# Performance work log

Hardware: AMD Instinct MI355X
Metric: run time of the kernel (lower is better)

Reference implementation:

```python
import jax, jax.numpy as jnp
import numpy as np

B, M, RPI = 16, 80, 256            # images, objects/image, relations/image
N, R = B * M, B * RPI
DF, REP, EMB, HID, NH, L = 12544, 1024, 256, 512, 8, 4
OBJC, RELC = 151, 51
IMW, IMH = 800.0, 600.0


def _ln(x, g, b):
    m = x.mean(-1, keepdims=True)
    v = ((x - m) ** 2).mean(-1, keepdims=True)
    return (x - m) * jax.lax.rsqrt(v + 1e-5) * g + b


def _encoder(x, qkv_w, qkv_b, out_w, out_b, f1_w, f1_b, f2_w, f2_b, ln1_s, ln1_b, ln2_s, ln2_b):
    # post-LN transformer encoder, L layers, x: [B, M, HID]
    Bb, Mm, D = x.shape
    dk = D // NH
    scale = 1.0 / jnp.sqrt(jnp.float32(dk))
    for l in range(L):
        qkv = x @ qkv_w[l].T + qkv_b[l]
        q, k, v = jnp.split(qkv, 3, axis=-1)
        hs = lambda t: t.reshape(Bb, Mm, NH, dk).transpose(0, 2, 1, 3)
        q, k, v = hs(q), hs(k), hs(v)
        att = jax.nn.softmax(jnp.einsum('bhqd,bhkd->bhqk', q, k) * scale, axis=-1)
        o = jnp.einsum('bhqk,bhkd->bhqd', att, v).transpose(0, 2, 1, 3).reshape(Bb, Mm, D)
        x = _ln(x + o @ out_w[l].T + out_b[l], ln1_s[l], ln1_b[l])
        f = jax.nn.relu(x @ f1_w[l].T + f1_b[l]) @ f2_w[l].T + f2_b[l]
        x = _ln(x + f, ln2_s[l], ln2_b[l])
    return x


def _box_info(boxes):
    wh = boxes[:, 2:] - boxes[:, :2] + 1.0
    xy = boxes[:, :2] + 0.5 * wh
    w, h = wh[:, :1], wh[:, 1:]
    x, y = xy[:, :1], xy[:, 1:]
    x1, y1, x2, y2 = boxes[:, 0:1], boxes[:, 1:2], boxes[:, 2:3], boxes[:, 3:4]
    return jnp.concatenate([w / IMW, h / IMH, x / IMW, y / IMH, x1 / IMW, y1 / IMH,
                            x2 / IMW, y2 / IMH, w * h / (IMW * IMH)], axis=-1)  # [N, 9]


def setup_inputs() -> dict:
    key = jax.random.key(0)
    ks = iter(jax.random.split(key, 80))
    nrm = lambda shape, s=0.02: jax.random.normal(next(ks), shape, jnp.float32) * s
    d = {}
    d['features'] = jax.random.normal(next(ks), (N, DF), jnp.float32)
    d['union_features'] = jax.random.normal(next(ks), (R, REP), jnp.float32)
    x1 = jax.random.uniform(next(ks), (N, 1)) * (IMW - 120.0)
    y1 = jax.random.uniform(next(ks), (N, 1)) * (IMH - 120.0)
    w = jax.random.uniform(next(ks), (N, 1)) * 100.0 + 5.0
    h = jax.random.uniform(next(ks), (N, 1)) * 100.0 + 5.0
    d['boxes'] = jnp.concatenate([x1, y1, x1 + w, y1 + h], axis=-1)
    d['logits'] = jax.random.normal(next(ks), (N, OBJC), jnp.float32)
    d['labels'] = jax.random.randint(next(ks), (N,), 0, OBJC)
    d['rel_pair_idxs'] = jax.random.randint(next(ks), (B, RPI, 2), 0, M)
    # feature extractor
    d['fe1_w'] = nrm((REP, DF)); d['fe1_b'] = jnp.zeros((REP,))
    d['fe2_w'] = nrm((REP, REP)); d['fe2_b'] = jnp.zeros((REP,))
    # embeddings
    d['emb1'] = nrm((OBJC, EMB), 1.0)
    d['emb2'] = nrm((OBJC, EMB), 1.0)
    # bbox embed 9->32->128
    d['bb1_w'] = nrm((32, 9)); d['bb1_b'] = jnp.zeros((32,))
    d['bb2_w'] = nrm((128, 32)); d['bb2_b'] = jnp.zeros((128,))
    d['lobj_w'] = nrm((HID, REP + EMB + 128)); d['lobj_b'] = jnp.zeros((HID,))
    d['ledge_w'] = nrm((HID, EMB + HID)); d['ledge_b'] = jnp.zeros((HID,))
    for p in ('o', 'e'):
        d[p + 'qkv_w'] = nrm((L, 3 * HID, HID)); d[p + 'qkv_b'] = jnp.zeros((L, 3 * HID))
        d[p + 'out_w'] = nrm((L, HID, HID)); d[p + 'out_b'] = jnp.zeros((L, HID))
        d[p + 'f1_w'] = nrm((L, HID, HID)); d[p + 'f1_b'] = jnp.zeros((L, HID))
        d[p + 'f2_w'] = nrm((L, HID, HID)); d[p + 'f2_b'] = jnp.zeros((L, HID))
        d[p + 'ln1_s'] = jnp.ones((L, HID)); d[p + 'ln1_b'] = jnp.zeros((L, HID))
        d[p + 'ln2_s'] = jnp.ones((L, HID)); d[p + 'ln2_b'] = jnp.zeros((L, HID))
    d['pcat_w'] = nrm((REP, 2 * HID)); d['pcat_b'] = jnp.zeros((REP,))
    d['fuse_w'] = nrm((REP, REP + HID)); d['fuse_b'] = jnp.zeros((REP,))
    d['cpx_w'] = nrm((RELC, 2 * REP)); d['cpx_b'] = jnp.zeros((RELC,))
    d['dpath_w'] = nrm((RELC, REP)); d['dpath_b'] = jnp.zeros((RELC,))
    return d


def reference(features, union_features, boxes, logits,
              fe1_w, fe1_b, fe2_w, fe2_b, emb1, emb2,
              bb1_w, bb1_b, bb2_w, bb2_b, lobj_w, lobj_b, ledge_w, ledge_b,
              oqkv_w, oqkv_b, oout_w, oout_b, of1_w, of1_b, of2_w, of2_b,
              oln1_s, oln1_b, oln2_s, oln2_b,
              eqkv_w, eqkv_b, eout_w, eout_b, ef1_w, ef1_b, ef2_w, ef2_b,
              eln1_s, eln1_b, eln2_s, eln2_b,
              pcat_w, pcat_b, fuse_w, fuse_b, cpx_w, cpx_b, dpath_w, dpath_b,
              labels, rel_pair_idxs):
    # FeatureExtractor
    bf = jax.nn.relu(features @ fe1_w.T + fe1_b)
    bf = jax.nn.relu(bf @ fe2_w.T + fe2_b)                        # [N, REP]
    # bbox embedding (dropout = identity in eval)
    pos = jax.nn.relu(_box_info(boxes) @ bb1_w.T + bb1_b)
    pos = jax.nn.relu(pos @ bb2_w.T + bb2_b)                      # [N, 128]
    obj_rep = jnp.concatenate([bf, emb1[labels], pos], -1) @ lobj_w.T + lobj_b  # [N, HID]
    obj_emb = _encoder(obj_rep.reshape(B, M, HID), oqkv_w, oqkv_b, oout_w, oout_b,
                       of1_w, of1_b, of2_w, of2_b, oln1_s, oln1_b, oln2_s, oln2_b)  # [B, M, HID]
    edge_in = jnp.concatenate([obj_emb.reshape(N, HID), emb2[labels]], -1) @ ledge_w.T + ledge_b
    gctx = _encoder(edge_in.reshape(B, M, HID), eqkv_w, eqkv_b, eout_w, eout_b,
                    ef1_w, ef1_b, ef2_w, ef2_b, eln1_s, eln1_b, eln2_s, eln2_b).mean(axis=1)  # [B, HID]
    # pair gather per image
    head = jax.vmap(lambda e, i: e[i])(obj_emb, rel_pair_idxs[:, :, 0])  # [B, RPI, HID]
    tail = jax.vmap(lambda e, i: e[i])(obj_emb, rel_pair_idxs[:, :, 1])
    pair = jnp.concatenate([head, tail], -1).reshape(R, 2 * HID)
    local = pair @ pcat_w.T + pcat_b                               # [R, REP]
    gexp = jnp.repeat(gctx, RPI, axis=0)                           # [R, HID]
    sem = jax.nn.relu(jnp.concatenate([local, gexp], -1) @ fuse_w.T + fuse_b)
    final = jnp.concatenate([sem, union_features], -1)             # [R, 2*REP]
    rel_logits = final @ cpx_w.T + cpx_b + local @ dpath_w.T + dpath_b  # [R, RELC]
    return rel_logits
```

## Files before the change

### kernel.cpp

```cpp
#include <hip/hip_runtime.h>
#include <hip/hip_bf16.h>
#include <cstdint>

#define DEV_INLINE __device__ __forceinline__

using u16 = unsigned short;
typedef __attribute__((ext_vector_type(8))) short bf8_t;
typedef __attribute__((ext_vector_type(4))) float f32x4;

constexpr int cB = 16, cM = 80, cRPI = 256;
constexpr int cN = cB * cM;
constexpr int cR = cB * cRPI;
constexpr int cDF = 12544, cREP = 1024, cEMB = 256, cHID = 512, cNH = 8, cL = 4;
constexpr int cRELC = 51;

DEV_INLINE u16 f2bf(float x) { return __builtin_bit_cast(u16, __float2bfloat16(x)); }
DEV_INLINE float bf2f(u16 u) { return __bfloat162float(__builtin_bit_cast(__hip_bfloat16, u)); }

DEV_INLINE float wave_max(float v) {
#pragma unroll
  for (int o = 32; o; o >>= 1) v = fmaxf(v, __shfl_xor(v, o));
  return v;
}
DEV_INLINE float wave_sum(float v) {
#pragma unroll
  for (int o = 32; o; o >>= 1) v += __shfl_xor(v, o);
  return v;
}

DEV_INLINE void xcd_remap(int& bx, int& by) {
  const int gx = gridDim.x;
  const int nwg = gx * gridDim.y;
  const int id = blockIdx.x + gx * blockIdx.y;
  const int q = nwg >> 3, r = nwg & 7;
  const int x = id & 7, k = id >> 3;
  const int idp = (x < r) ? x * (q + 1) + k : r * (q + 1) + (x - r) * q + k;
  bx = idp % gx;
  by = idp / gx;
}

template <int KK>
__global__ __launch_bounds__(256) void gemm_k1(
    const u16* __restrict__ A, int lda,
    const u16* __restrict__ Bw, int ldb,
    float* __restrict__ outF, int ldc,
    u16* __restrict__ outH, int ldh,
    const float* __restrict__ bias,
    const float* __restrict__ res, int resld, int resmode,
    int relu)
{
  constexpr int GR = KK / 8;
  constexpr int CH = 32 * GR;
  __shared__ u16 As[32 * KK];
  __shared__ u16 Bs[32 * KK];
  const int tid = threadIdx.x;
  const int wid = tid >> 6, lane = tid & 63;
  const int l15 = lane & 15, l4 = lane >> 4;
  int bx, by;
  xcd_remap(bx, by);
  const int bm = by * 32, bn = bx * 32;
  const int wr = wid >> 1, wc = wid & 1;

#pragma unroll
  for (int i = 0; i < CH / 256; ++i) {
    const int c = i * 256 + tid;
    const int row = c / GR, gran = c % GR;
    const int sg = gran ^ (row & 7);
    const u16* gp = A + (size_t)(bm + row) * lda + sg * 8;
    __builtin_amdgcn_global_load_lds(
        (const __attribute__((address_space(1))) void*)gp,
        (__attribute__((address_space(3))) void*)((char*)As + (size_t)(i * 256 + wid * 64) * 16),
        16, 0, 0);
  }
#pragma unroll
  for (int i = 0; i < CH / 256; ++i) {
    const int c = i * 256 + tid;
    const int row = c / GR, gran = c % GR;
    const int sg = gran ^ (row & 7);
    const u16* gp = Bw + (size_t)(bn + row) * ldb + sg * 8;
    __builtin_amdgcn_global_load_lds(
        (const __attribute__((address_space(1))) void*)gp,
        (__attribute__((address_space(3))) void*)((char*)Bs + (size_t)(i * 256 + wid * 64) * 16),
        16, 0, 0);
  }
  __syncthreads();

  const int ra = wr * 16 + l15;
  const int rb = wc * 16 + l15;
  f32x4 acc = {};
#pragma unroll
  for (int ks = 0; ks < KK / 32; ++ks) {
    const int ga = ((ks << 2) | l4) ^ (ra & 7);
    const int gb = ((ks << 2) | l4) ^ (rb & 7);
    const bf8_t af = *(const bf8_t*)&As[ra * KK + ga * 8];
    const bf8_t bv = *(const bf8_t*)&Bs[rb * KK + gb * 8];
    acc = __builtin_amdgcn_mfma_f32_16x16x32_bf16(af, bv, acc, 0, 0, 0);
  }

  const int ccol = bn + wc * 16 + l15;
  const float bv = bias ? bias[ccol] : 0.f;
#pragma unroll
  for (int g = 0; g < 4; ++g) {
    const int r = bm + wr * 16 + l4 * 4 + g;
    float v = acc[g] + bv;
    if (resmode == 1) v += res[(size_t)r * resld + ccol];
    else if (resmode == 2) v += res[(size_t)(r >> 8) * resld + ccol];
    if (relu) v = fmaxf(v, 0.f);
    if (outF) outF[(size_t)r * ldc + ccol] = v;
    if (outH) outH[(size_t)r * ldh + ccol] = f2bf(v);
  }
}

static void g512(hipStream_t s, const u16* A, int lda, const u16* W, int ldb,
                 int M, int N, float* outF, int ldc, u16* outH, int ldh,
                 const float* bias, const float* res, int resld, int resmode, int relu) {
  dim3 g(N / 32, M / 32);
  gemm_k1<512><<<g, 256, 0, s>>>(A, lda, W, ldb, outF, ldc, outH, ldh,
                                 bias, res, resld, resmode, relu);
}

template <int BM, int BN, bool SPLIT>
__global__ __launch_bounds__(256) void gemm_h(
    const u16* __restrict__ A, int lda,
    const u16* __restrict__ Bw, int ldb,
    int Mr, int Nr, int Klen,
    float* __restrict__ outF, int ldc,
    u16* __restrict__ outH, int ldh,
    const float* __restrict__ bias,
    const float* __restrict__ res, int resld, int resmode,
    int relu)
{
  constexpr int MF = BM > 32 ? BM / 32 : 1, NF = BN > 32 ? BN / 32 : 1;
  constexpr int ACH = BM * 4, BCH = BN * 4;
  __shared__ u16 As[2][BM * 32];
  __shared__ u16 Bs[2][BN * 32];
  const int tid = threadIdx.x;
  const int wid = tid >> 6, lane = tid & 63;
  const int l15 = lane & 15, l4 = lane >> 4;
  int bx, by;
  xcd_remap(bx, by);
  const int bm = by * BM, bn = bx * BN;
  const int wr = wid >> 1, wc = wid & 1;
  const int kbase = SPLIT ? blockIdx.z * Klen : 0;

  f32x4 acc[MF][NF] = {};

  auto stage = [&](int buf, int ks) {
    const int k0 = kbase + (ks << 5);
#pragma unroll
    for (int i = 0; i < (ACH + 255) / 256; ++i) {
      const int cA = i * 256 + tid;
      if (ACH % 256 == 0 || cA < ACH) {
        const int row = cA >> 2, seg = cA & 3;
        const int sseg = seg ^ (row & 3);
        const u16* gp = A + (size_t)(bm + row) * lda + k0 + sseg * 8;
        __builtin_amdgcn_global_load_lds(
            (const __attribute__((address_space(1))) void*)gp,
            (__attribute__((address_space(3))) void*)((char*)As[buf] + (size_t)(cA - lane) * 16),
            16, 0, 0);
      }
    }
#pragma unroll
    for (int i = 0; i < (BCH + 255) / 256; ++i) {
      const int cBp = i * 256 + ((tid + 128) & 255);
      if (BCH % 256 == 0 || cBp < BCH) {
        const int row = cBp >> 2, seg = cBp & 3;
        const int sseg = seg ^ (row & 3);
        int brow = bn + row; if (brow > Nr - 1) brow = Nr - 1;
        const u16* gp = Bw + (size_t)brow * ldb + k0 + sseg * 8;
        __builtin_amdgcn_global_load_lds(
            (const __attribute__((address_space(1))) void*)gp,
            (__attribute__((address_space(3))) void*)((char*)Bs[buf] + (size_t)(cBp - lane) * 16),
            16, 0, 0);
      }
    }
  };

  const int nk = Klen >> 5;
  stage(0, 0);
  __syncthreads();

  for (int ks = 0; ks < nk; ++ks) {
    const int cur = ks & 1;
    if (ks + 1 < nk) stage(cur ^ 1, ks + 1);

    bf8_t af[MF], bfr[NF];
#pragma unroll
    for (int m = 0; m < MF; ++m) {
      const int r = wr * (BM / 2) + m * 16 + l15;
      const int g = l4 ^ (r & 3);
      af[m] = *(const bf8_t*)&As[cur][r * 32 + g * 8];
    }
#pragma unroll
    for (int n = 0; n < NF; ++n) {
      const int r = wc * (BN / 2) + n * 16 + l15;
      const int g = l4 ^ (r & 3);
      bfr[n] = *(const bf8_t*)&Bs[cur][r * 32 + g * 8];
    }
#pragma unroll
    for (int m = 0; m < MF; ++m)
#pragma unroll
      for (int n = 0; n < NF; ++n)
        acc[m][n] = __builtin_amdgcn_mfma_f32_16x16x32_bf16(af[m], bfr[n], acc[m][n], 0, 0, 0);
    __syncthreads();
  }

  if (SPLIT) {
    float* po = outF + (size_t)blockIdx.z * Mr * ldc;
#pragma unroll
    for (int m = 0; m < MF; ++m)
#pragma unroll
      for (int n = 0; n < NF; ++n) {
        const int ccol = bn + wc * (BN / 2) + n * 16 + l15;
        if (ccol >= Nr) continue;
#pragma unroll
        for (int g = 0; g < 4; ++g) {
          const int r = bm + wr * (BM / 2) + m * 16 + l4 * 4 + g;
          po[(size_t)r * ldc + ccol] = acc[m][n][g];
        }
      }
  } else {
#pragma unroll
    for (int m = 0; m < MF; ++m)
#pragma unroll
      for (int n = 0; n < NF; ++n) {
        const int ccol = bn + wc * (BN / 2) + n * 16 + l15;
        if (ccol >= Nr) continue;
        const float bv = bias ? bias[ccol] : 0.f;
#pragma unroll
        for (int g = 0; g < 4; ++g) {
          const int r = bm + wr * (BM / 2) + m * 16 + l4 * 4 + g;
          float v = acc[m][n][g] + bv;
          if (resmode == 1) v += res[(size_t)r * resld + ccol];
          else if (resmode == 2) v += res[(size_t)(r >> 8) * resld + ccol];
          if (relu) v = fmaxf(v, 0.f);
          if (outF) outF[(size_t)r * ldc + ccol] = v;
          if (outH) outH[(size_t)r * ldh + ccol] = f2bf(v);
        }
      }
  }
}

template <int BM, int BN>
static void g16(hipStream_t s, const u16* A, int lda, const u16* W, int ldb,
                int M, int N, int K, float* outF, int ldc, u16* outH, int ldh,
                const float* bias, const float* res, int resld, int resmode, int relu) {
  dim3 g((N + BN - 1) / BN, M / BM);
  gemm_h<BM, BN, false><<<g, 256, 0, s>>>(A, lda, W, ldb, M, N, K, outF, ldc, outH, ldh,
                                          bias, res, resld, resmode, relu);
}

__global__ void conv_big2(const float* __restrict__ f, const float* __restrict__ w,
                          u16* __restrict__ fh, u16* __restrict__ wh) {
  constexpr int N1 = cN * cDF / 4;
  constexpr int N2 = cREP * cDF / 4;
  for (int i = blockIdx.x * 256 + threadIdx.x; i < N1 + N2; i += gridDim.x * 256) {
    const float4 v = (i < N1) ? ((const float4*)f)[i] : ((const float4*)w)[i - N1];
    ushort4 o = {f2bf(v.x), f2bf(v.y), f2bf(v.z), f2bf(v.w)};
    if (i < N1) ((ushort4*)fh)[i] = o; else ((ushort4*)wh)[i - N1] = o;
  }
}

constexpr size_t W_FE2 = 0, W_LOBJ = W_FE2 + 1048576, W_LEDGE = W_LOBJ + 720896,
  W_OQKV = W_LEDGE + 393216, W_OOUT = W_OQKV + 3145728, W_OF1 = W_OOUT + 1048576,
  W_OF2 = W_OF1 + 1048576, W_EQKV = W_OF2 + 1048576, W_EOUT = W_EQKV + 3145728,
  W_EF1 = W_EOUT + 1048576, W_EF2 = W_EF1 + 1048576, W_PCAT = W_EF2 + 1048576,
  W_FUSE = W_PCAT + 1048576, W_WEND = W_FUSE + 1572864;

struct EncSrcs {
  const float *fe2, *lobj, *ledge, *oqkv, *oout, *of1, *of2,
              *eqkv, *eout, *ef1, *ef2, *pcat, *fuse;
};

__global__ void conv_enc(EncSrcs S, u16* __restrict__ wb) {
#define SEG(nm, OFF, PRE, LEN) \
  if (i < (PRE) + (LEN)) { \
    const float4 v = ((const float4*)S.nm)[i - (PRE)]; \
    ushort4 o = {f2bf(v.x), f2bf(v.y), f2bf(v.z), f2bf(v.w)}; \
    ((ushort4*)(wb + (OFF)))[i - (PRE)] = o; \
  } else
  for (int i = blockIdx.x * 256 + threadIdx.x; i < (int)(W_WEND / 4); i += gridDim.x * 256) {
    SEG(fe2,  W_FE2,   0,       262144)
    SEG(lobj, W_LOBJ,  262144,  180224)
    SEG(ledge,W_LEDGE, 442368,  98304)
    SEG(oqkv, W_OQKV,  540672,  786432)
    SEG(oout, W_OOUT,  1327104, 262144)
    SEG(of1,  W_OF1,   1589248, 262144)
    SEG(of2,  W_OF2,   1851392, 262144)
    SEG(eqkv, W_EQKV,  2113536, 786432)
    SEG(eout, W_EOUT,  2899968, 262144)
    SEG(ef1,  W_EF1,   3162112, 262144)
    SEG(ef2,  W_EF2,   3424256, 262144)
    SEG(pcat, W_PCAT,  3686400, 262144)
    SEG(fuse, W_FUSE,  3948544, 393216)
    { }
  }
#undef SEG
}

__global__ void conv_cat(const float* __restrict__ cpx, const float* __restrict__ dpath,
                         const float* __restrict__ cb, const float* __restrict__ db,
                         u16* __restrict__ catw, float* __restrict__ biasc) {
  constexpr int N1 = cRELC * 512;
  constexpr int N2 = cRELC * 256;
  const int i0 = blockIdx.x * 256 + threadIdx.x;
  if (blockIdx.x == 0 && threadIdx.x < cRELC) biasc[threadIdx.x] = cb[threadIdx.x] + db[threadIdx.x];
  for (int i = i0; i < N1 + N2; i += gridDim.x * 256) {
    if (i < N1) {
      const int r = i >> 9, c = i & 511;
      const float4 v = ((const float4*)cpx)[i];
      ushort4 o = {f2bf(v.x), f2bf(v.y), f2bf(v.z), f2bf(v.w)};
      ((ushort4*)catw)[r * 768 + c] = o;
    } else {
      const int j = i - N1, r = j >> 8, c = j & 255;
      const float4 v = ((const float4*)dpath)[j];
      ushort4 o = {f2bf(v.x), f2bf(v.y), f2bf(v.z), f2bf(v.w)};
      ((ushort4*)catw)[r * 768 + 512 + c] = o;
    }
  }
}

__global__ void conv2d_kernel(const float* __restrict__ src, int slda,
                              u16* __restrict__ dst, int dld, int cols) {
  const int r = blockIdx.x;
  for (int c = threadIdx.x; c < cols; c += blockDim.x)
    dst[(size_t)r * dld + c] = f2bf(src[(size_t)r * slda + c]);
}

__global__ __launch_bounds__(256) void prep_obj(
    const float* __restrict__ boxes,
    const float* __restrict__ bb1w, const float* __restrict__ bb1b,
    const float* __restrict__ bb2w, const float* __restrict__ bb2b,
    const float* __restrict__ emb1, const int* __restrict__ labels,
    u16* __restrict__ obj_in) {
  __shared__ float W1[288];
  __shared__ float W2[4096];
  __shared__ float P1[8][33];
  const int tid = threadIdx.x;
  for (int i = tid; i < 288; i += 256) W1[i] = bb1w[i];
  for (int i = tid; i < 4096; i += 256) W2[i] = bb2w[i];
  __syncthreads();
  const int r8 = tid >> 5, sub = tid & 31;
  const int row = blockIdx.x * 8 + r8;
  const float x1 = boxes[row * 4], y1 = boxes[row * 4 + 1];
  const float x2 = boxes[row * 4 + 2], y2 = boxes[row * 4 + 3];
  const float w = x2 - x1 + 1.f, h = y2 - y1 + 1.f;
  const float bi[9] = {w / 800.f, h / 600.f, (x1 + 0.5f * w) / 800.f, (y1 + 0.5f * h) / 600.f,
                       x1 / 800.f, y1 / 600.f, x2 / 800.f, y2 / 600.f, w * h / 480000.f};
  float p = bb1b[sub];
#pragma unroll
  for (int j = 0; j < 9; ++j) p += bi[j] * W1[sub * 9 + j];
  P1[r8][sub] = fmaxf(p, 0.f);
  __syncthreads();
#pragma unroll
  for (int jo = 0; jo < 4; ++jo) {
    const int o = sub + jo * 32;
    float a = bb2b[o];
#pragma unroll
    for (int j2 = 0; j2 < 32; ++j2) a += P1[r8][j2] * W2[o * 32 + j2];
    obj_in[(size_t)row * 1408 + 1280 + o] = f2bf(fmaxf(a, 0.f));
  }
  const int l = labels[row];
#pragma unroll
  for (int k = 0; k < 8; ++k)
    obj_in[(size_t)row * 1408 + 1024 + sub + k * 32] = f2bf(emb1[(size_t)l * 256 + sub + k * 32]);
}

__global__ void gather_emb_h(const float* __restrict__ emb, const int* __restrict__ labels,
                             u16* __restrict__ dst, int dld) {
  const int i = blockIdx.x;
  const int l = labels[i];
  const float* s = emb + (size_t)l * cEMB;
  for (int c = threadIdx.x; c < cEMB; c += blockDim.x)
    dst[(size_t)i * dld + c] = f2bf(s[c]);
}

__global__ __launch_bounds__(256) void attn_kernel(const u16* __restrict__ qkv,
                                                   u16* __restrict__ o) {
  __shared__ float Ks[80][65];
  __shared__ float Vs[80][65];
  const int bh = blockIdx.x;
  const int b = bh >> 3, h = bh & 7;
  const int tid = threadIdx.x;
  const u16* base = qkv + (size_t)(b * cM) * 1536 + h * 64;

  for (int e = tid; e < 640; e += 256) {
    const int r = e >> 3, d0 = (e & 7) * 8;
    const bf8_t kv = *(const bf8_t*)&base[(size_t)r * 1536 + 512 + d0];
    const bf8_t vv = *(const bf8_t*)&base[(size_t)r * 1536 + 1024 + d0];
#pragma unroll
    for (int j = 0; j < 8; ++j) {
      Ks[r][d0 + j] = bf2f((u16)kv[j]);
      Vs[r][d0 + j] = bf2f((u16)vv[j]);
    }
  }
  __syncthreads();

  const int wave = tid >> 6, lane = tid & 63;
  const int r0 = blockIdx.y * 16;
  for (int r = r0 + wave; r < r0 + 16; r += 4) {
    const float qd = bf2f(base[(size_t)r * 1536 + lane]);
    const int c2 = 64 + lane;
    const int c2c = (c2 < 80) ? c2 : 0;
    float s0 = 0.f, s1 = 0.f;
#pragma unroll 8
    for (int d = 0; d < 64; ++d) {
      const float qv = __shfl(qd, d);
      s0 += qv * Ks[lane][d];
      s1 += qv * Ks[c2c][d];
    }
    s0 *= 0.125f;
    s1 = (c2 < 80) ? s1 * 0.125f : -1e30f;
    const float mx = wave_max(fmaxf(s0, s1));
    const float p0 = __expf(s0 - mx);
    const float p1 = (c2 < 80) ? __expf(s1 - mx) : 0.f;
    const float ssum = wave_sum(p0 + p1);

    float od = 0.f;
#pragma unroll 8
    for (int c = 0; c < 64; ++c) od += __shfl(p0, c) * Vs[c][lane];
#pragma unroll
    for (int c = 0; c < 16; ++c) od += __shfl(p1, c) * Vs[64 + c][lane];
    od /= ssum;
    o[(size_t)(b * cM + r) * cHID + h * 64 + lane] = f2bf(od);
  }
}

__global__ __launch_bounds__(256) void ln_kernel(
    const float* __restrict__ in, float* __restrict__ outF,
    u16* __restrict__ outH, int ldh,
    const float* __restrict__ g, const float* __restrict__ bta) {
  const int row = blockIdx.x * 4 + (threadIdx.x >> 6);
  const int lane = threadIdx.x & 63;
  const float* x = in + (size_t)row * cHID;
  float v[8];
  float s = 0.f;
#pragma unroll
  for (int i = 0; i < 8; ++i) { v[i] = x[lane + i * 64]; s += v[i]; }
  s = wave_sum(s);
  const float mean = s * (1.f / 512.f);
  float vs = 0.f;
#pragma unroll
  for (int i = 0; i < 8; ++i) { const float d = v[i] - mean; vs += d * d; }
  vs = wave_sum(vs);
  const float inv = rsqrtf(vs * (1.f / 512.f) + 1e-5f);
#pragma unroll
  for (int i = 0; i < 8; ++i) {
    const int c = lane + i * 64;
    const float y = (v[i] - mean) * inv * g[c] + bta[c];
    outF[(size_t)row * cHID + c] = y;
    outH[(size_t)row * ldh + c] = f2bf(y);
  }
}

__global__ void mean_kernel(const float* __restrict__ x, u16* __restrict__ gctx_h) {
  const int b = blockIdx.x;
  const int c = threadIdx.x;
  float s = 0.f;
  for (int m = 0; m < cM; ++m) s += x[(size_t)(b * cM + m) * cHID + c];
  gctx_h[(size_t)b * cHID + c] = f2bf(s * (1.f / 80.f));
}

__global__ void pair_gather_h(const u16* __restrict__ obj, int old, const int* __restrict__ idx,
                              u16* __restrict__ pair) {
  const int r = blockIdx.x;
  const int b = r >> 8, rr = r & 255;
  const int i0 = idx[(size_t)(b * cRPI + rr) * 2 + 0];
  const int i1 = idx[(size_t)(b * cRPI + rr) * 2 + 1];
  const u16* hsrc = obj + (size_t)(b * cM + i0) * old;
  const u16* tsrc = obj + (size_t)(b * cM + i1) * old;
  u16* p = pair + (size_t)r * 1024;
  for (int c = threadIdx.x; c < cHID; c += blockDim.x) {
    p[c] = hsrc[c];
    p[cHID + c] = tsrc[c];
  }
}

__global__ void reduce8_kernel(const float* __restrict__ p, const float* __restrict__ bias,
                               u16* __restrict__ outH) {
  const int idx = blockIdx.x * 256 + threadIdx.x;
  constexpr int total = cN * cREP;
  if (idx >= total) return;
  float v = bias[idx & 1023];
#pragma unroll
  for (int z = 0; z < 8; ++z) v += p[(size_t)z * total + idx];
  outH[idx] = f2bf(fmaxf(v, 0.f));
}

__global__ void freduce_kernel(const float* __restrict__ p, const float* __restrict__ biasc,
                               float* __restrict__ out) {
  const int idx = blockIdx.x * 256 + threadIdx.x;
  if (idx >= cR * cRELC) return;
  const int r = idx / cRELC, c = idx - r * cRELC;
  float v = biasc[c];
#pragma unroll
  for (int z = 0; z < 4; ++z) v += p[(size_t)z * cR * 64 + (size_t)r * 64 + c];
  out[idx] = v;
}

static void run_encoder(hipStream_t s, float* x, u16* xh, u16* qkvh, u16* attn_h,
                        float* res1, u16* f_h,
                        const u16* qkvw, const float* qkvb,
                        const u16* outw, const float* outb,
                        const u16* f1w, const float* f1b,
                        const u16* f2w, const float* f2b,
                        const float* ln1s, const float* ln1b,
                        const float* ln2s, const float* ln2b,
                        u16* last_bf, int last_ld) {
  for (int l = 0; l < cL; ++l) {
    g512(s, xh, 512, qkvw + (size_t)l * 1536 * 512, 512, cN, 1536,
         nullptr, 0, qkvh, 1536, qkvb + l * 1536, nullptr, 0, 0, 0);
    attn_kernel<<<dim3(cB * cNH, 5), 256, 0, s>>>(qkvh, attn_h);
    g512(s, attn_h, 512, outw + (size_t)l * 512 * 512, 512, cN, 512,
         res1, 512, nullptr, 0, outb + l * 512, x, 512, 1, 0);
    ln_kernel<<<cN / 4, 256, 0, s>>>(res1, x, xh, 512, ln1s + l * 512, ln1b + l * 512);
    g512(s, xh, 512, f1w + (size_t)l * 512 * 512, 512, cN, 512,
         nullptr, 0, f_h, 512, f1b + l * 512, nullptr, 0, 0, 1);
    g512(s, f_h, 512, f2w + (size_t)l * 512 * 512, 512, cN, 512,
         res1, 512, nullptr, 0, f2b + l * 512, x, 512, 1, 0);
    const bool last = (l == cL - 1);
    ln_kernel<<<cN / 4, 256, 0, s>>>(res1, x, last ? last_bf : xh, last ? last_ld : 512,
                                     ln2s + l * 512, ln2b + l * 512);
  }
}

constexpr size_t OFF_FEAT  = 0;
constexpr size_t OFF_FE1W  = 32112640;
constexpr size_t OFF_PART  = 57802752;
constexpr size_t P_END     = 99745792;
constexpr size_t OFF_PAIR  = 0;
constexpr size_t OFF_FINAL = 8388608;
constexpr size_t OFF_OBJIN = 33554432;
constexpr size_t OFF_QKVH  = 37158912;
constexpr size_t OFF_X     = 41091072;
constexpr size_t OFF_XH    = 43712512;
constexpr size_t OFF_ATTN  = 45023232;
constexpr size_t OFF_RES   = 46333952;
constexpr size_t OFF_FH    = 48955392;
constexpr size_t OFF_EDGE  = 50266112;

extern "C" void kernel_launch(void* const* d_in, const int* in_sizes, int n_in,
                              void* d_out, int out_size, void* d_ws, size_t ws_size,
                              hipStream_t stream) {
  (void)in_sizes; (void)n_in; (void)out_size; (void)ws_size;

  const float* features = (const float*)d_in[0];
  const float* unionf   = (const float*)d_in[1];
  const float* boxes    = (const float*)d_in[2];
  const int*   labels   = (const int*)d_in[4];
  const int*   relidx   = (const int*)d_in[5];
  const float* fe1_w = (const float*)d_in[6];
  const float* fe1_b = (const float*)d_in[7];
  const float* fe2_w = (const float*)d_in[8];
  const float* fe2_b = (const float*)d_in[9];
  const float* emb1  = (const float*)d_in[10];
  const float* emb2  = (const float*)d_in[11];
  const float* bb1_w = (const float*)d_in[12];
  const float* bb1_b = (const float*)d_in[13];
  const float* bb2_w = (const float*)d_in[14];
  const float* bb2_b = (const float*)d_in[15];
  const float* lobj_w = (const float*)d_in[16];
  const float* lobj_b = (const float*)d_in[17];
  const float* ledge_w = (const float*)d_in[18];
  const float* ledge_b = (const float*)d_in[19];
  const float* oqkv_w = (const float*)d_in[20];
  const float* oqkv_b = (const float*)d_in[21];
  const float* oout_w = (const float*)d_in[22];
  const float* oout_b = (const float*)d_in[23];
  const float* of1_w = (const float*)d_in[24];
  const float* of1_b = (const float*)d_in[25];
  const float* of2_w = (const float*)d_in[26];
  const float* of2_b = (const float*)d_in[27];
  const float* oln1_s = (const float*)d_in[28];
  const float* oln1_b = (const float*)d_in[29];
  const float* oln2_s = (const float*)d_in[30];
  const float* oln2_b = (const float*)d_in[31];
  const float* eqkv_w = (const float*)d_in[32];
  const float* eqkv_b = (const float*)d_in[33];
  const float* eout_w = (const float*)d_in[34];
  const float* eout_b = (const float*)d_in[35];
  const float* ef1_w = (const float*)d_in[36];
  const float* ef1_b = (const float*)d_in[37];
  const float* ef2_w = (const float*)d_in[38];
  const float* ef2_b = (const float*)d_in[39];
  const float* eln1_s = (const float*)d_in[40];
  const float* eln1_b = (const float*)d_in[41];
  const float* eln2_s = (const float*)d_in[42];
  const float* eln2_b = (const float*)d_in[43];
  const float* pcat_w = (const float*)d_in[44];
  const float* pcat_b = (const float*)d_in[45];
  const float* fuse_w = (const float*)d_in[46];
  const float* fuse_b = (const float*)d_in[47];
  const float* cpx_w  = (const float*)d_in[48];
  const float* cpx_b  = (const float*)d_in[49];
  const float* dpath_w = (const float*)d_in[50];
  const float* dpath_b = (const float*)d_in[51];

  char* wsb = (char*)d_ws;
  u16* feat_h  = (u16*)(wsb + OFF_FEAT);
  u16* fe1w_h  = (u16*)(wsb + OFF_FE1W);
  float* part  = (float*)(wsb + OFF_PART);
  u16* pair    = (u16*)(wsb + OFF_PAIR);
  u16* finalb  = (u16*)(wsb + OFF_FINAL);
  u16* obj_in  = (u16*)(wsb + OFF_OBJIN);
  u16* qkvh    = (u16*)(wsb + OFF_QKVH);
  float* x     = (float*)(wsb + OFF_X);
  u16* xh      = (u16*)(wsb + OFF_XH);
  u16* attn_h  = (u16*)(wsb + OFF_ATTN);
  float* res1  = (float*)(wsb + OFF_RES);
  u16* f_h     = (u16*)(wsb + OFF_FH);
  u16* edge_in = (u16*)(wsb + OFF_EDGE);

  size_t off = P_END;
  auto alloc = [&](size_t bytes) { char* p = wsb + off; off = (off + bytes + 255) & ~(size_t)255; return p; };
  u16* wblock   = (u16*)alloc(W_WEND * 2);
  u16* catw     = (u16*)alloc(313344);
  float* biasc  = (float*)alloc(256);
  u16* bf0h     = (u16*)alloc(2621440);
  u16* gctx_h   = (u16*)alloc(65536);
  float* gcproj = (float*)alloc(262144);
  float* fpart  = (float*)alloc(4194304);

  const u16* fe2w_h   = wblock + W_FE2;
  const u16* lobjw_h  = wblock + W_LOBJ;
  const u16* ledgew_h = wblock + W_LEDGE;
  const u16* oqkvw_h  = wblock + W_OQKV;
  const u16* ooutw_h  = wblock + W_OOUT;
  const u16* of1w_h   = wblock + W_OF1;
  const u16* of2w_h   = wblock + W_OF2;
  const u16* eqkvw_h  = wblock + W_EQKV;
  const u16* eoutw_h  = wblock + W_EOUT;
  const u16* ef1w_h   = wblock + W_EF1;
  const u16* ef2w_h   = wblock + W_EF2;
  const u16* pcatw_h  = wblock + W_PCAT;
  const u16* fusew_h  = wblock + W_FUSE;

  conv_big2<<<2048, 256, 0, stream>>>(features, fe1_w, feat_h, fe1w_h);
  EncSrcs es = {fe2_w, lobj_w, ledge_w, oqkv_w, oout_w, of1_w, of2_w,
                eqkv_w, eout_w, ef1_w, ef2_w, pcat_w, fuse_w};
  conv_enc<<<2048, 256, 0, stream>>>(es, wblock);
  conv_cat<<<160, 256, 0, stream>>>(cpx_w, dpath_w, cpx_b, dpath_b, catw, biasc);

  gemm_h<128, 128, true><<<dim3(8, 10, 8), 256, 0, stream>>>(
      feat_h, cDF, fe1w_h, cDF, cN, cREP, cDF / 8, part, cREP,
      nullptr, 0, nullptr, nullptr, 0, 0, 0);
  reduce8_kernel<<<(cN * cREP + 255) / 256, 256, 0, stream>>>(part, fe1_b, bf0h);

  prep_obj<<<cN / 8, 256, 0, stream>>>(boxes, bb1_w, bb1_b, bb2_w, bb2_b, emb1, labels, obj_in);

  g16<32, 32>(stream, bf0h, 1024, fe2w_h, 1024, cN, cREP, cREP,
              nullptr, 0, obj_in, 1408, fe2_b, nullptr, 0, 0, 1);

  g16<32, 32>(stream, obj_in, 1408, lobjw_h, 1408, cN, cHID, 1408,
              x, 512, xh, 512, lobj_b, nullptr, 0, 0, 0);

  run_encoder(stream, x, xh, qkvh, attn_h, res1, f_h,
              oqkvw_h, oqkv_b, ooutw_h, oout_b, of1w_h, of1_b, of2w_h, of2_b,
              oln1_s, oln1_b, oln2_s, oln2_b, edge_in, 768);

  gather_emb_h<<<cN, 256, 0, stream>>>(emb2, labels, edge_in + 512, 768);
  pair_gather_h<<<cR, 256, 0, stream>>>(edge_in, 768, relidx, pair);

  g16<32, 32>(stream, edge_in, 768, ledgew_h, 768, cN, cHID, 768,
              x, 512, xh, 512, ledge_b, nullptr, 0, 0, 0);
  run_encoder(stream, x, xh, qkvh, attn_h, res1, f_h,
              eqkvw_h, eqkv_b, eoutw_h, eout_b, ef1w_h, ef1_b, ef2w_h, ef2_b,
              eln1_s, eln1_b, eln2_s, eln2_b, xh, 512);
  mean_kernel<<<cB, cHID, 0, stream>>>(x, gctx_h);

  g512(stream, gctx_h, 512, fusew_h + 1024, 1536, 64, cREP,
       gcproj, 1024, nullptr, 0, fuse_b, nullptr, 0, 0, 0);

  conv2d_kernel<<<cR, 256, 0, stream>>>(unionf, 1024, finalb + 1024, 3072, 1024);
  g16<128, 64>(stream, pair, 1024, pcatw_h, 1024, cR, cREP, 1024,
               nullptr, 0, finalb + 2048, 3072, pcat_b, nullptr, 0, 0, 0);
  g16<128, 64>(stream, finalb + 2048, 3072, fusew_h, 1536, cR, cREP, 1024,
               nullptr, 0, finalb, 3072, nullptr, gcproj, 1024, 2, 1);

  gemm_h<64, 64, true><<<dim3(1, 64, 4), 256, 0, stream>>>(
      finalb, 3072, catw, 3072, cR, cRELC, 3072 / 4, fpart, 64,
      nullptr, 0, nullptr, nullptr, 0, 0, 0);
  freduce_kernel<<<(cR * cRELC + 255) / 256, 256, 0, stream>>>(fpart, biasc, (float*)d_out);
}
```

Measured before the change: 879.7 us.

## Fuse LayerNorm into encoder GEMMs and merge conversion and gather kernels

Adds a gemm_ln kernel that applies LayerNorm on the fly, either normalizing the A operand (with per-row stats computed in-kernel) or normalizing the residual in the epilogue. The encoder no longer launches separate ln_kernel passes except at the last layer, and it shifts the next layer's QKV projection to consume the LN2 output directly. It also merges the three weight/feature conversion kernels into one launch, and the embedding gather with the pair gather. This is meant to cut launch count and the round trips of normalized activations through memory. The cost is that LN statistics are recomputed per column-tile block, using a one-pass variance formula.

```diff
diff --git a/kernel.cpp b/kernel.cpp
--- a/kernel.cpp
+++ b/kernel.cpp
@@ -26,6 +26,12 @@
 #pragma unroll
   for (int o = 32; o; o >>= 1) v += __shfl_xor(v, o);
   return v;
+}
+
+DEV_INLINE void gl_lds16(const u16* gp, char* lp) {
+  __builtin_amdgcn_global_load_lds(
+      (const __attribute__((address_space(1))) void*)gp,
+      (__attribute__((address_space(3))) void*)lp, 16, 0, 0);
 }
 
 DEV_INLINE void xcd_remap(int& bx, int& by) {
@@ -37,6 +43,129 @@
   const int idp = (x < r) ? x * (q + 1) + k : r * (q + 1) + (x - r) * q + k;
   bx = idp % gx;
   by = idp / gx;
+}
+
+template <int LNA, int LNRES>
+__global__ __launch_bounds__(256) void gemm_ln(
+    const u16* __restrict__ Ah,
+    const float* __restrict__ Sres,
+    const float* __restrict__ lnS, const float* __restrict__ lnB,
+    const u16* __restrict__ W,
+    float* __restrict__ outF,
+    u16* __restrict__ outH, int ldh,
+    const float* __restrict__ bias, int relu)
+{
+  __shared__ u16 As[32 * 512];
+  __shared__ u16 Bs[32 * 512];
+  __shared__ float stat[32][2];
+  const int tid = threadIdx.x;
+  const int wid = tid >> 6, lane = tid & 63;
+  const int l15 = lane & 15, l4 = lane >> 4;
+  int bx, by;
+  xcd_remap(bx, by);
+  const int bm = by * 32, bn = bx * 32;
+  const int wr = wid >> 1, wc = wid & 1;
+
+#pragma unroll
+  for (int i = 0; i < 8; ++i) {
+    const int c = i * 256 + tid;
+    const int row = c >> 6, gran = c & 63;
+    const int sg = gran ^ (row & 7);
+    gl_lds16(W + (size_t)(bn + row) * 512 + sg * 8,
+             (char*)Bs + (size_t)(i * 256 + wid * 64) * 16);
+  }
+
+  if (LNA) {
+    const int r8 = tid >> 3, sub = tid & 7;
+    const float4* rp4 = (const float4*)(Sres + (size_t)(bm + r8) * 512 + sub * 64);
+    float4 v[16];
+    float s = 0.f, q = 0.f;
+#pragma unroll
+    for (int k = 0; k < 16; ++k) {
+      v[k] = rp4[k];
+      s += v[k].x + v[k].y + v[k].z + v[k].w;
+      q += v[k].x * v[k].x + v[k].y * v[k].y + v[k].z * v[k].z + v[k].w * v[k].w;
+    }
+#pragma unroll
+    for (int o = 1; o < 8; o <<= 1) { s += __shfl_xor(s, o); q += __shfl_xor(q, o); }
+    const float mean = s * (1.f / 512.f);
+    const float inv = rsqrtf(q * (1.f / 512.f) - mean * mean + 1e-5f);
+    if (sub == 0) { stat[r8][0] = mean; stat[r8][1] = inv; }
+    const float4* ls4 = (const float4*)(lnS + sub * 64);
+    const float4* lb4 = (const float4*)(lnB + sub * 64);
+#pragma unroll
+    for (int k2 = 0; k2 < 8; ++k2) {
+      const float4 a = v[k2 * 2], b = v[k2 * 2 + 1];
+      const float4 sa = ls4[k2 * 2], sb = ls4[k2 * 2 + 1];
+      const float4 ba = lb4[k2 * 2], bb = lb4[k2 * 2 + 1];
+      bf8_t wv;
+      wv[0] = (short)f2bf((a.x - mean) * inv * sa.x + ba.x);
+      wv[1] = (short)f2bf((a.y - mean) * inv * sa.y + ba.y);
+      wv[2] = (short)f2bf((a.z - mean) * inv * sa.z + ba.z);
+      wv[3] = (short)f2bf((a.w - mean) * inv * sa.w + ba.w);
+      wv[4] = (short)f2bf((b.x - mean) * inv * sb.x + bb.x);
+      wv[5] = (short)f2bf((b.y - mean) * inv * sb.y + bb.y);
+      wv[6] = (short)f2bf((b.z - mean) * inv * sb.z + bb.z);
+      wv[7] = (short)f2bf((b.w - mean) * inv * sb.w + bb.w);
+      const int g = sub * 8 + k2;
+      const int sg = g ^ (r8 & 7);
+      *(bf8_t*)&As[r8 * 512 + sg * 8] = wv;
+    }
+  } else {
+#pragma unroll
+    for (int i = 0; i < 8; ++i) {
+      const int c = i * 256 + tid;
+      const int row = c >> 6, gran = c & 63;
+      const int sg = gran ^ (row & 7);
+      gl_lds16(Ah + (size_t)(bm + row) * 512 + sg * 8,
+               (char*)As + (size_t)(i * 256 + wid * 64) * 16);
+    }
+    if (LNRES) {
+      const int r8 = tid >> 3, sub = tid & 7;
+      const float4* rp4 = (const float4*)(Sres + (size_t)(bm + r8) * 512 + sub * 64);
+      float s = 0.f, q = 0.f;
+#pragma unroll
+      for (int k = 0; k < 16; ++k) {
+        const float4 t = rp4[k];
+        s += t.x + t.y + t.z + t.w;
+        q += t.x * t.x + t.y * t.y + t.z * t.z + t.w * t.w;
+      }
+#pragma unroll
+      for (int o = 1; o < 8; o <<= 1) { s += __shfl_xor(s, o); q += __shfl_xor(q, o); }
+      const float mean = s * (1.f / 512.f);
+      const float inv = rsqrtf(q * (1.f / 512.f) - mean * mean + 1e-5f);
+      if (sub == 0) { stat[r8][0] = mean; stat[r8][1] = inv; }
+    }
+  }
+  __syncthreads();
+
+  const int ra = wr * 16 + l15;
+  const int rbr = wc * 16 + l15;
+  f32x4 acc = {};
+#pragma unroll
+  for (int ks = 0; ks < 16; ++ks) {
+    const int ga = ((ks << 2) | l4) ^ (ra & 7);
+    const int gb = ((ks << 2) | l4) ^ (rbr & 7);
+    const bf8_t af = *(const bf8_t*)&As[ra * 512 + ga * 8];
+    const bf8_t bv = *(const bf8_t*)&Bs[rbr * 512 + gb * 8];
+    acc = __builtin_amdgcn_mfma_f32_16x16x32_bf16(af, bv, acc, 0, 0, 0);
+  }
+
+  const int ccol = bn + wc * 16 + l15;
+  const float bv = bias[ccol];
+  float rs = 0.f, rbb = 0.f;
+  if (LNRES) { rs = lnS[ccol]; rbb = lnB[ccol]; }
+#pragma unroll
+  for (int g = 0; g < 4; ++g) {
+    const int rl = wr * 16 + l4 * 4 + g;
+    const int r = bm + rl;
+    float vv = acc[g] + bv;
+    if (LNRES)
+      vv += (Sres[(size_t)r * 512 + ccol] - stat[rl][0]) * stat[rl][1] * rs + rbb;
+    if (relu) vv = fmaxf(vv, 0.f);
+    if (outF) outF[(size_t)r * 512 + ccol] = vv;
+    if (outH) outH[(size_t)r * ldh + ccol] = f2bf(vv);
+  }
 }
 
 template <int KK>
@@ -66,22 +195,16 @@
     const int c = i * 256 + tid;
     const int row = c / GR, gran = c % GR;
     const int sg = gran ^ (row & 7);
-    const u16* gp = A + (size_t)(bm + row) * lda + sg * 8;
-    __builtin_amdgcn_global_load_lds(
-        (const __attribute__((address_space(1))) void*)gp,
-        (__attribute__((address_space(3))) void*)((char*)As + (size_t)(i * 256 + wid * 64) * 16),
-        16, 0, 0);
+    gl_lds16(A + (size_t)(bm + row) * lda + sg * 8,
+             (char*)As + (size_t)(i * 256 + wid * 64) * 16);
   }
 #pragma unroll
   for (int i = 0; i < CH / 256; ++i) {
     const int c = i * 256 + tid;
     const int row = c / GR, gran = c % GR;
     const int sg = gran ^ (row & 7);
-    const u16* gp = Bw + (size_t)(bn + row) * ldb + sg * 8;
-    __builtin_amdgcn_global_load_lds(
-        (const __attribute__((address_space(1))) void*)gp,
-        (__attribute__((address_space(3))) void*)((char*)Bs + (size_t)(i * 256 + wid * 64) * 16),
-        16, 0, 0);
+    gl_lds16(Bw + (size_t)(bn + row) * ldb + sg * 8,
+             (char*)Bs + (size_t)(i * 256 + wid * 64) * 16);
   }
   __syncthreads();
 
@@ -153,11 +276,8 @@
       if (ACH % 256 == 0 || cA < ACH) {
         const int row = cA >> 2, seg = cA & 3;
         const int sseg = seg ^ (row & 3);
-        const u16* gp = A + (size_t)(bm + row) * lda + k0 + sseg * 8;
-        __builtin_amdgcn_global_load_lds(
-            (const __attribute__((address_space(1))) void*)gp,
-            (__attribute__((address_space(3))) void*)((char*)As[buf] + (size_t)(cA - lane) * 16),
-            16, 0, 0);
+        gl_lds16(A + (size_t)(bm + row) * lda + k0 + sseg * 8,
+                 (char*)As[buf] + (size_t)(cA - lane) * 16);
       }
     }
 #pragma unroll
@@ -167,11 +287,8 @@
         const int row = cBp >> 2, seg = cBp & 3;
         const int sseg = seg ^ (row & 3);
         int brow = bn + row; if (brow > Nr - 1) brow = Nr - 1;
-        const u16* gp = Bw + (size_t)brow * ldb + k0 + sseg * 8;
-        __builtin_amdgcn_global_load_lds(
-            (const __attribute__((address_space(1))) void*)gp,
-            (__attribute__((address_space(3))) void*)((char*)Bs[buf] + (size_t)(cBp - lane) * 16),
-            16, 0, 0);
+        gl_lds16(Bw + (size_t)brow * ldb + k0 + sseg * 8,
+                 (char*)Bs[buf] + (size_t)(cBp - lane) * 16);
       }
     }
   };
@@ -250,74 +367,61 @@
                                           bias, res, resld, resmode, relu);
 }
 
-__global__ void conv_big2(const float* __restrict__ f, const float* __restrict__ w,
-                          u16* __restrict__ fh, u16* __restrict__ wh) {
-  constexpr int N1 = cN * cDF / 4;
-  constexpr int N2 = cREP * cDF / 4;
-  for (int i = blockIdx.x * 256 + threadIdx.x; i < N1 + N2; i += gridDim.x * 256) {
-    const float4 v = (i < N1) ? ((const float4*)f)[i] : ((const float4*)w)[i - N1];
-    ushort4 o = {f2bf(v.x), f2bf(v.y), f2bf(v.z), f2bf(v.w)};
-    if (i < N1) ((ushort4*)fh)[i] = o; else ((ushort4*)wh)[i - N1] = o;
-  }
-}
-
 constexpr size_t W_FE2 = 0, W_LOBJ = W_FE2 + 1048576, W_LEDGE = W_LOBJ + 720896,
   W_OQKV = W_LEDGE + 393216, W_OOUT = W_OQKV + 3145728, W_OF1 = W_OOUT + 1048576,
   W_OF2 = W_OF1 + 1048576, W_EQKV = W_OF2 + 1048576, W_EOUT = W_EQKV + 3145728,
   W_EF1 = W_EOUT + 1048576, W_EF2 = W_EF1 + 1048576, W_PCAT = W_EF2 + 1048576,
   W_FUSE = W_PCAT + 1048576, W_WEND = W_FUSE + 1572864;
 
-struct EncSrcs {
+struct ConvAll {
+  const float *features, *fe1w;
   const float *fe2, *lobj, *ledge, *oqkv, *oout, *of1, *of2,
               *eqkv, *eout, *ef1, *ef2, *pcat, *fuse;
+  const float *cpx, *dpath, *cb, *db;
+  u16 *feat_h, *fe1w_h, *wb, *catw;
+  float *biasc;
 };
 
-__global__ void conv_enc(EncSrcs S, u16* __restrict__ wb) {
-#define SEG(nm, OFF, PRE, LEN) \
+__global__ void conv_all(ConvAll C) {
+  if (blockIdx.x == 0 && threadIdx.x < cRELC)
+    C.biasc[threadIdx.x] = C.cb[threadIdx.x] + C.db[threadIdx.x];
+#define CSEG(src, dst, PRE, LEN) \
   if (i < (PRE) + (LEN)) { \
-    const float4 v = ((const float4*)S.nm)[i - (PRE)]; \
+    const float4 v = ((const float4*)(src))[i - (PRE)]; \
     ushort4 o = {f2bf(v.x), f2bf(v.y), f2bf(v.z), f2bf(v.w)}; \
-    ((ushort4*)(wb + (OFF)))[i - (PRE)] = o; \
+    ((ushort4*)(dst))[i - (PRE)] = o; \
   } else
-  for (int i = blockIdx.x * 256 + threadIdx.x; i < (int)(W_WEND / 4); i += gridDim.x * 256) {
-    SEG(fe2,  W_FE2,   0,       262144)
-    SEG(lobj, W_LOBJ,  262144,  180224)
-    SEG(ledge,W_LEDGE, 442368,  98304)
-    SEG(oqkv, W_OQKV,  540672,  786432)
-    SEG(oout, W_OOUT,  1327104, 262144)
-    SEG(of1,  W_OF1,   1589248, 262144)
-    SEG(of2,  W_OF2,   1851392, 262144)
-    SEG(eqkv, W_EQKV,  2113536, 786432)
-    SEG(eout, W_EOUT,  2899968, 262144)
-    SEG(ef1,  W_EF1,   3162112, 262144)
-    SEG(ef2,  W_EF2,   3424256, 262144)
-    SEG(pcat, W_PCAT,  3686400, 262144)
-    SEG(fuse, W_FUSE,  3948544, 393216)
-    { }
-  }
-#undef SEG
-}
-
-__global__ void conv_cat(const float* __restrict__ cpx, const float* __restrict__ dpath,
-                         const float* __restrict__ cb, const float* __restrict__ db,
-                         u16* __restrict__ catw, float* __restrict__ biasc) {
-  constexpr int N1 = cRELC * 512;
-  constexpr int N2 = cRELC * 256;
-  const int i0 = blockIdx.x * 256 + threadIdx.x;
-  if (blockIdx.x == 0 && threadIdx.x < cRELC) biasc[threadIdx.x] = cb[threadIdx.x] + db[threadIdx.x];
-  for (int i = i0; i < N1 + N2; i += gridDim.x * 256) {
-    if (i < N1) {
-      const int r = i >> 9, c = i & 511;
-      const float4 v = ((const float4*)cpx)[i];
+  for (int i = blockIdx.x * 256 + threadIdx.x; i < 11606272; i += gridDim.x * 256) {
+    CSEG(C.features, C.feat_h,      0,        4014080)
+    CSEG(C.fe1w,     C.fe1w_h,      4014080,  3211264)
+    CSEG(C.fe2,      C.wb + W_FE2,  7225344,  262144)
+    CSEG(C.lobj,     C.wb + W_LOBJ, 7487488,  180224)
+    CSEG(C.ledge,    C.wb + W_LEDGE,7667712,  98304)
+    CSEG(C.oqkv,     C.wb + W_OQKV, 7766016,  786432)
+    CSEG(C.oout,     C.wb + W_OOUT, 8552448,  262144)
+    CSEG(C.of1,      C.wb + W_OF1,  8814592,  262144)
+    CSEG(C.of2,      C.wb + W_OF2,  9076736,  262144)
+    CSEG(C.eqkv,     C.wb + W_EQKV, 9338880,  786432)
+    CSEG(C.eout,     C.wb + W_EOUT, 10125312, 262144)
+    CSEG(C.ef1,      C.wb + W_EF1,  10387456, 262144)
+    CSEG(C.ef2,      C.wb + W_EF2,  10649600, 262144)
+    CSEG(C.pcat,     C.wb + W_PCAT, 10911744, 262144)
+    CSEG(C.fuse,     C.wb + W_FUSE, 11173888, 393216)
+    if (i < 11593216) {
+      const int j = i - 11567104;
+      const int r = j >> 9, c = j & 511;
+      const float4 v = ((const float4*)C.cpx)[j];
       ushort4 o = {f2bf(v.x), f2bf(v.y), f2bf(v.z), f2bf(v.w)};
-      ((ushort4*)catw)[r * 768 + c] = o;
+      ((ushort4*)C.catw)[r * 768 + c] = o;
     } else {
-      const int j = i - N1, r = j >> 8, c = j & 255;
-      const float4 v = ((const float4*)dpath)[j];
+      const int j = i - 11593216;
+      const int r = j >> 8, c = j & 255;
+      const float4 v = ((const float4*)C.dpath)[j];
       ushort4 o = {f2bf(v.x), f2bf(v.y), f2bf(v.z), f2bf(v.w)};
-      ((ushort4*)catw)[r * 768 + 512 + c] = o;
-    }
-  }
+      ((ushort4*)C.catw)[r * 768 + 512 + c] = o;
+    }
+  }
+#undef CSEG
 }
 
 __global__ void conv2d_kernel(const float* __restrict__ src, int slda,
@@ -366,13 +470,25 @@
     obj_in[(size_t)row * 1408 + 1024 + sub + k * 32] = f2bf(emb1[(size_t)l * 256 + sub + k * 32]);
 }
 
-__global__ void gather_emb_h(const float* __restrict__ emb, const int* __restrict__ labels,
-                             u16* __restrict__ dst, int dld) {
-  const int i = blockIdx.x;
-  const int l = labels[i];
-  const float* s = emb + (size_t)l * cEMB;
-  for (int c = threadIdx.x; c < cEMB; c += blockDim.x)
-    dst[(size_t)i * dld + c] = f2bf(s[c]);
+__global__ void gather_pair(const float* __restrict__ emb2, const int* __restrict__ labels,
+                            u16* __restrict__ edge_in,
+                            const int* __restrict__ idx, u16* __restrict__ pair) {
+  const int r = blockIdx.x;
+  const int tid = threadIdx.x;
+  if (r < cN && tid < cEMB) {
+    const int l = labels[r];
+    edge_in[(size_t)r * 768 + 512 + tid] = f2bf(emb2[(size_t)l * cEMB + tid]);
+  }
+  const int b = r >> 8, rr = r & 255;
+  const int i0 = idx[(size_t)(b * cRPI + rr) * 2 + 0];
+  const int i1 = idx[(size_t)(b * cRPI + rr) * 2 + 1];
+  const u16* hsrc = edge_in + (size_t)(b * cM + i0) * 768;
+  const u16* tsrc = edge_in + (size_t)(b * cM + i1) * 768;
+  u16* p = pair + (size_t)r * 1024;
+  for (int c = tid; c < cHID; c += blockDim.x) {
+    p[c] = hsrc[c];
+    p[cHID + c] = tsrc[c];
+  }
 }
 
 __global__ __launch_bounds__(256) void attn_kernel(const u16* __restrict__ qkv,
@@ -461,21 +577,6 @@
   gctx_h[(size_t)b * cHID + c] = f2bf(s * (1.f / 80.f));
 }
 
-__global__ void pair_gather_h(const u16* __restrict__ obj, int old, const int* __restrict__ idx,
-                              u16* __restrict__ pair) {
-  const int r = blockIdx.x;
-  const int b = r >> 8, rr = r & 255;
-  const int i0 = idx[(size_t)(b * cRPI + rr) * 2 + 0];
-  const int i1 = idx[(size_t)(b * cRPI + rr) * 2 + 1];
-  const u16* hsrc = obj + (size_t)(b * cM + i0) * old;
-  const u16* tsrc = obj + (size_t)(b * cM + i1) * old;
-  u16* p = pair + (size_t)r * 1024;
-  for (int c = threadIdx.x; c < cHID; c += blockDim.x) {
-    p[c] = hsrc[c];
-    p[cHID + c] = tsrc[c];
-  }
-}
-
 __global__ void reduce8_kernel(const float* __restrict__ p, const float* __restrict__ bias,
                                u16* __restrict__ outH) {
   const int idx = blockIdx.x * 256 + threadIdx.x;
@@ -499,7 +600,7 @@
 }
 
 static void run_encoder(hipStream_t s, float* x, u16* xh, u16* qkvh, u16* attn_h,
-                        float* res1, u16* f_h,
+                        float* res1, float* res2, u16* f_h,
                         const u16* qkvw, const float* qkvb,
                         const u16* outw, const float* outb,
                         const u16* f1w, const float* f1b,
@@ -507,20 +608,28 @@
                         const float* ln1s, const float* ln1b,
                         const float* ln2s, const float* ln2b,
                         u16* last_bf, int last_ld) {
+  g512(s, xh, 512, qkvw, 512, cN, 1536, nullptr, 0, qkvh, 1536, qkvb, nullptr, 0, 0, 0);
   for (int l = 0; l < cL; ++l) {
-    g512(s, xh, 512, qkvw + (size_t)l * 1536 * 512, 512, cN, 1536,
-         nullptr, 0, qkvh, 1536, qkvb + l * 1536, nullptr, 0, 0, 0);
     attn_kernel<<<dim3(cB * cNH, 5), 256, 0, s>>>(qkvh, attn_h);
-    g512(s, attn_h, 512, outw + (size_t)l * 512 * 512, 512, cN, 512,
-         res1, 512, nullptr, 0, outb + l * 512, x, 512, 1, 0);
-    ln_kernel<<<cN / 4, 256, 0, s>>>(res1, x, xh, 512, ln1s + l * 512, ln1b + l * 512);
-    g512(s, xh, 512, f1w + (size_t)l * 512 * 512, 512, cN, 512,
-         nullptr, 0, f_h, 512, f1b + l * 512, nullptr, 0, 0, 1);
-    g512(s, f_h, 512, f2w + (size_t)l * 512 * 512, 512, cN, 512,
-         res1, 512, nullptr, 0, f2b + l * 512, x, 512, 1, 0);
-    const bool last = (l == cL - 1);
-    ln_kernel<<<cN / 4, 256, 0, s>>>(res1, x, last ? last_bf : xh, last ? last_ld : 512,
-                                     ln2s + l * 512, ln2b + l * 512);
+    if (l == 0)
+      g512(s, attn_h, 512, outw, 512, cN, 512, res1, 512, nullptr, 0, outb, x, 512, 1, 0);
+    else
+      gemm_ln<0, 1><<<dim3(16, 40), 256, 0, s>>>(
+          attn_h, res2, ln2s + (l - 1) * 512, ln2b + (l - 1) * 512,
+          outw + (size_t)l * 512 * 512, res1, nullptr, 512, outb + l * 512, 0);
+    gemm_ln<1, 0><<<dim3(16, 40), 256, 0, s>>>(
+        nullptr, res1, ln1s + l * 512, ln1b + l * 512,
+        f1w + (size_t)l * 512 * 512, nullptr, f_h, 512, f1b + l * 512, 1);
+    gemm_ln<0, 1><<<dim3(16, 40), 256, 0, s>>>(
+        f_h, res1, ln1s + l * 512, ln1b + l * 512,
+        f2w + (size_t)l * 512 * 512, res2, nullptr, 512, f2b + l * 512, 0);
+    if (l < cL - 1)
+      gemm_ln<1, 0><<<dim3(48, 40), 256, 0, s>>>(
+          nullptr, res2, ln2s + l * 512, ln2b + l * 512,
+          qkvw + (size_t)(l + 1) * 1536 * 512, nullptr, qkvh, 1536, qkvb + (l + 1) * 1536, 0);
+    else
+      ln_kernel<<<cN / 4, 256, 0, s>>>(res2, x, last_bf, last_ld,
+                                       ln2s + l * 512, ln2b + l * 512);
   }
 }
 
@@ -538,6 +647,7 @@
 constexpr size_t OFF_RES   = 46333952;
 constexpr size_t OFF_FH    = 48955392;
 constexpr size_t OFF_EDGE  = 50266112;
+constexpr size_t OFF_RES2  = 52232192;
 
 extern "C" void kernel_launch(void* const* d_in, const int* in_sizes, int n_in,
                               void* d_out, int out_size, void* d_ws, size_t ws_size,
@@ -610,6 +720,7 @@
   float* res1  = (float*)(wsb + OFF_RES);
   u16* f_h     = (u16*)(wsb + OFF_FH);
   u16* edge_in = (u16*)(wsb + OFF_EDGE);
+  float* res2  = (float*)(wsb + OFF_RES2);
 
   size_t off = P_END;
   auto alloc = [&](size_t bytes) { char* p = wsb + off; off = (off + bytes + 255) & ~(size_t)255; return p; };
@@ -624,22 +735,15 @@
   const u16* fe2w_h   = wblock + W_FE2;
   const u16* lobjw_h  = wblock + W_LOBJ;
   const u16* ledgew_h = wblock + W_LEDGE;
-  const u16* oqkvw_h  = wblock + W_OQKV;
-  const u16* ooutw_h  = wblock + W_OOUT;
-  const u16* of1w_h   = wblock + W_OF1;
-  const u16* of2w_h   = wblock + W_OF2;
-  const u16* eqkvw_h  = wblock + W_EQKV;
-  const u16* eoutw_h  = wblock + W_EOUT;
-  const u16* ef1w_h   = wblock + W_EF1;
-  const u16* ef2w_h   = wblock + W_EF2;
   const u16* pcatw_h  = wblock + W_PCAT;
   const u16* fusew_h  = wblock + W_FUSE;
 
-  conv_big2<<<2048, 256, 0, stream>>>(features, fe1_w, feat_h, fe1w_h);
-  EncSrcs es = {fe2_w, lobj_w, ledge_w, oqkv_w, oout_w, of1_w, of2_w,
-                eqkv_w, eout_w, ef1_w, ef2_w, pcat_w, fuse_w};
-  conv_enc<<<2048, 256, 0, stream>>>(es, wblock);
-  conv_cat<<<160, 256, 0, stream>>>(cpx_w, dpath_w, cpx_b, dpath_b, catw, biasc);
+  ConvAll ca = {features, fe1_w,
+                fe2_w, lobj_w, ledge_w, oqkv_w, oout_w, of1_w, of2_w,
+                eqkv_w, eout_w, ef1_w, ef2_w, pcat_w, fuse_w,
+                cpx_w, dpath_w, cpx_b, dpath_b,
+                feat_h, fe1w_h, wblock, catw, biasc};
+  conv_all<<<2048, 256, 0, stream>>>(ca);
 
   gemm_h<128, 128, true><<<dim3(8, 10, 8), 256, 0, stream>>>(
       feat_h, cDF, fe1w_h, cDF, cN, cREP, cDF / 8, part, cREP,
@@ -654,17 +758,18 @@
   g16<32, 32>(stream, obj_in, 1408, lobjw_h, 1408, cN, cHID, 1408,
               x, 512, xh, 512, lobj_b, nullptr, 0, 0, 0);
 
-  run_encoder(stream, x, xh, qkvh, attn_h, res1, f_h,
-              oqkvw_h, oqkv_b, ooutw_h, oout_b, of1w_h, of1_b, of2w_h, of2_b,
+  run_encoder(stream, x, xh, qkvh, attn_h, res1, res2, f_h,
+              wblock + W_OQKV, oqkv_b, wblock + W_OOUT, oout_b,
+              wblock + W_OF1, of1_b, wblock + W_OF2, of2_b,
               oln1_s, oln1_b, oln2_s, oln2_b, edge_in, 768);
 
-  gather_emb_h<<<cN, 256, 0, stream>>>(emb2, labels, edge_in + 512, 768);
-  pair_gather_h<<<cR, 256, 0, stream>>>(edge_in, 768, relidx, pair);
+  gather_pair<<<cR, 256, 0, stream>>>(emb2, labels, edge_in, relidx, pair);
 
   g16<32, 32>(stream, edge_in, 768, ledgew_h, 768, cN, cHID, 768,
               x, 512, xh, 512, ledge_b, nullptr, 0, 0, 0);
-  run_encoder(stream, x, xh, qkvh, attn_h, res1, f_h,
-              eqkvw_h, eqkv_b, eoutw_h, eout_b, ef1w_h, ef1_b, ef2w_h, ef2_b,
+  run_encoder(stream, x, xh, qkvh, attn_h, res1, res2, f_h,
+              wblock + W_EQKV, eqkv_b, wblock + W_EOUT, eout_b,
+              wblock + W_EF1, ef1_b, wblock + W_EF2, ef2_b,
               eln1_s, eln1_b, eln2_s, eln2_b, xh, 512);
   mean_kernel<<<cB, cHID, 0, stream>>>(x, gctx_h);
 
```

Result: slower. 1.181 ms (+34.2%).
